# Performance work log

Hardware: AMD Instinct MI355X
Metric: run time of the kernel (lower is better)

The kernel has to match this reference:

```python
import jax, jax.numpy as jnp
import numpy as np
import math

B, SEQ, E, H, NB, NHYP = 4, 1024, 512, 8, 64, 6
V, HID, NC, ENC = 32000, 2048, 6, 6
DH = E // H


def _pos_encoding(n, e, dtype):
    pos = jnp.arange(n, dtype=dtype)[:, None]
    div = jnp.exp(-jnp.arange(0, e, 2, dtype=dtype) * (math.log(10000.0) / e))
    ang = pos * div  # [n, e/2]
    pe = jnp.zeros((n, e), dtype)
    pe = pe.at[:, 0::2].set(jnp.sin(ang))
    pe = pe.at[:, 1::2].set(jnp.cos(ang))
    return pe


def _layer_norm(x, g, b):
    m = x.mean(-1, keepdims=True)
    v = ((x - m) ** 2).mean(-1, keepdims=True)
    return (x - m) / jnp.sqrt(v + 1e-5) * g + b


def _lsh_attention(x, Wq, bq, Wv, bv, hyper):
    b, n, e = x.shape
    q = x @ Wq + bq
    v = x @ Wv + bv
    q4 = q.reshape(b, n, H, DH)  # [b,n,h,d]
    v4 = v.reshape(b, n, H, DH)
    # bucket hashing: append bias 1, project on hyperplanes, binarize, binary-encode
    aug = jnp.concatenate([q4, jnp.ones((b, n, H, 1), q.dtype)], axis=-1)
    proj = jnp.einsum('bnhe,ey->bnhy', aug, hyper)
    bits = (proj >= 0).astype(q.dtype)
    pows = (2 ** jnp.arange(NHYP)).astype(q.dtype)
    buckets = jnp.einsum('bnhy,y->bnh', bits, pows).astype(jnp.int32)
    bh = buckets.transpose(0, 2, 1)  # [b,h,n]
    qh = q4.transpose(0, 2, 1, 3)  # [b,h,n,d]
    vh = v4.transpose(0, 2, 1, 3)
    scores = jnp.einsum('bhnd,bhmd->bhnm', qh, qh) / math.sqrt(e)
    # torch code zeroes q rows at their OWN bucket and sums q_c @ q_c^T over all
    # NB buckets; that equals scores * (NB - 2 + [bucket_i == bucket_j]) exactly.
    same = bh[:, :, :, None] == bh[:, :, None, :]
    count = (NB - 2 + same.astype(jnp.int32)).astype(scores.dtype)
    attn = jax.nn.softmax(scores * count, axis=-1)
    out = jnp.einsum('bhnm,bhmd->bhnd', attn, vh)
    return out.transpose(0, 2, 1, 3).reshape(b, n, e)


def setup_inputs() -> dict:
    key = jax.random.key(0)
    ks = jax.random.split(key, 16)
    s = 0.02
    emb = jax.random.normal(ks[0], (V, E), jnp.float32) * s
    emb = emb.at[V - 1].set(0.0)  # padding_idx row
    return dict(
        inputs=jax.random.randint(ks[1], (B, SEQ), 0, V),
        emb=emb,
        gamma=jnp.ones((E,), jnp.float32),
        beta=jnp.zeros((E,), jnp.float32),
        Wq=jax.random.normal(ks[2], (E, E), jnp.float32) * s,
        bq=jnp.zeros((E,), jnp.float32),
        Wv=jax.random.normal(ks[3], (E, E), jnp.float32) * s,
        bv=jnp.zeros((E,), jnp.float32),
        hyper=jax.random.normal(ks[4], (DH + 1, NHYP), jnp.float32),
        W1=jax.random.normal(ks[5], (E, HID), jnp.float32) * s,
        b1=jnp.zeros((HID,), jnp.float32),
        W2=jax.random.normal(ks[6], (HID, E), jnp.float32) * s,
        b2=jnp.zeros((E,), jnp.float32),
        Wm=jax.random.normal(ks[7], (E * SEQ, NC), jnp.float32) * 0.002,
        bm=jnp.zeros((NC,), jnp.float32),
    )


def reference(inputs, emb, gamma, beta, Wq, bq, Wv, bv, hyper, W1, b1, W2, b2, Wm, bm):
    x = emb[inputs]  # [B, SEQ, E]
    x = x + _pos_encoding(x.shape[1], x.shape[2], x.dtype)
    for _ in range(ENC):  # shared weights across encoders
        a = _lsh_attention(x, Wq, bq, Wv, bv, hyper)
        x = _layer_norm(a, gamma, beta)
        x = jax.nn.relu(x @ W1 + b1) @ W2 + b2 + x
        x = _layer_norm(x, gamma, beta)
    x = x.reshape(x.shape[0], -1)
    return x @ Wm + bm  # [B, NC]
```

## Files before the change

kernel.cpp:

```cpp
#include <hip/hip_runtime.h>
#include <hip/hip_bf16.h>
#include <math.h>

#define B_    4
#define SEQ_  1024
#define E_    512
#define H_    8
#define DH_   64
#define NHYP_ 6
#define HID_  2048
#define NC_   6
#define ENC_  6
#define BH_   (B_*H_)
#define NTOK_ 4096
#define NCAT_ 1088

typedef __attribute__((ext_vector_type(8))) short short8;
typedef __attribute__((ext_vector_type(4))) float f32x4;

static __device__ __forceinline__ float wave_rsum(float v){
#pragma unroll
  for(int o=32;o;o>>=1) v += __shfl_down(v,o,64);
  return v;
}
static __device__ __forceinline__ ushort f2b(float v){
  __hip_bfloat16 h = __float2bfloat16(v);
  return *(ushort*)&h;
}
static __device__ __forceinline__ float b2f(ushort u){
  unsigned int x = ((unsigned int)u) << 16;
  return *(float*)&x;
}
static __device__ __forceinline__ void gload16(const void* g, void* l){
  __builtin_amdgcn_global_load_lds(
      (const __attribute__((address_space(1))) void*)g,
      (__attribute__((address_space(3))) void*)l,
      16, 0, 0);
}

__global__ void embed_pe_kernel(const int* __restrict__ inp, const float* __restrict__ emb,
                                float* __restrict__ x, ushort* __restrict__ xh,
                                unsigned int* __restrict__ MaxN){
  int row = blockIdx.x;
  if(blockIdx.x==0 && threadIdx.x<32) MaxN[threadIdx.x] = 0u;
  int s = row & (SEQ_-1);
  int idx = inp[row];
  const float* er = emb + (size_t)idx*E_;
  float* xr = x + (size_t)row*E_;
  ushort* hr = xh + (size_t)row*E_;
  for(int c=threadIdx.x;c<E_;c+=blockDim.x){
    int i = c>>1;
    float div = expf(-(float)i * 0.0359778920780319646f);
    float ang = (float)s * div;
    float pe = (c&1) ? cosf(ang) : sinf(ang);
    float v = er[c] + pe;
    xr[c] = v;
    hr[c] = f2b(v);
  }
}

__global__ __launch_bounds__(256) void prep_kernel(
    const float* __restrict__ Wq, const float* __restrict__ Wv,
    const float* __restrict__ W1, const float* __restrict__ W2,
    const float* __restrict__ bq, const float* __restrict__ bv,
    const float* __restrict__ hyper,
    ushort* __restrict__ WcatT, ushort* __restrict__ W1T,
    ushort* __restrict__ W2T, float* __restrict__ bcat)
{
  int bid = blockIdx.x;
  if(bid < 2560){
    const float* W; ushort* Wt; int K, N, tile;
    if(bid < 256){       W=Wq; Wt=WcatT;                    K=512;  N=512;  tile=bid; }
    else if(bid < 512){  W=Wv; Wt=WcatT+(size_t)512*512;    K=512;  N=512;  tile=bid-256; }
    else if(bid < 1536){ W=W1; Wt=W1T;                      K=512;  N=2048; tile=bid-512; }
    else {               W=W2; Wt=W2T;                      K=2048; N=512;  tile=bid-1536; }
    int tpr = N >> 5;
    int n0 = (tile % tpr)*32, k0 = (tile / tpr)*32;
    __shared__ float T[32][33];
    int tx = threadIdx.x & 31, ty = threadIdx.x >> 5;
#pragma unroll
    for(int i=0;i<32;i+=8) T[ty+i][tx] = W[(size_t)(k0+ty+i)*N + n0+tx];
    __syncthreads();
#pragma unroll
    for(int i=0;i<32;i+=8)
      Wt[(size_t)(n0+ty+i)*K + k0+tx] = f2b(T[tx][ty+i]);
  } else if(bid < 2688){
    int t = (bid-2560)*256 + threadIdx.x;
    int c = t >> 9, k = t & 511;
    float s = 0.f;
    if(c < 48){
      int h = c/6, y = c%6;
      const float* wr = Wq + (size_t)k*E_ + h*DH_;
      for(int d=0;d<DH_;++d) s += wr[d]*hyper[d*NHYP_+y];
    }
    WcatT[(size_t)(1024+c)*E_ + k] = f2b(s);
  } else {
    int t = (bid-2688)*256 + threadIdx.x;
    if(t >= NCAT_) return;
    float v;
    if(t < 512) v = bq[t];
    else if(t < 1024) v = bv[t-512];
    else if(t < 1072){
      int c = t - 1024, h = c/6, y = c%6;
      float s = hyper[DH_*NHYP_ + y];
      for(int d=0;d<DH_;++d) s += bq[h*DH_+d]*hyper[d*NHYP_+y];
      v = s;
    } else v = 0.f;
    bcat[t] = v;
  }
}

template<int BM, int BN, int EPI>
__global__ __launch_bounds__(256) void gemm_mfma(
    const ushort* __restrict__ A, const ushort* __restrict__ Bt,
    const float* __restrict__ bias, const float* __restrict__ res,
    void* __restrict__ C0, void* __restrict__ C1, void* __restrict__ C2,
    void* __restrict__ C3, int M, int N, int K)
{
  constexpr int MI = BM/32, NI = BN/32;
  constexpr int ACH = BM/32, BCH = BN/32;
  __shared__ ushort As[2][BM*64];
  __shared__ ushort Bs[2][BN*64];
  __shared__ float epi[64*49];
  int tid = threadIdx.x;
  int w = tid>>6, lane = tid&63, g = lane>>4, li = lane&15;
  int wr = w>>1, wc = w&1;
  int bm = blockIdx.y*BM, bn = blockIdx.x*BN;
  int kz = blockIdx.z;
  int kcnt = K / (int)gridDim.z;
  int kbase = kz * kcnt;
  int NK = kcnt >> 6;

  f32x4 acc[MI][NI] = {};

  auto issue = [&](int ks, int pb){
    int k0 = kbase + ks*64;
#pragma unroll
    for(int it=0; it<ACH; ++it){
      int c = it*256 + tid; int r = c>>3; int kq = ((c&7)^(r&7))*8;
      gload16(&A[(size_t)(bm+r)*K + k0 + kq], &As[pb][it*2048 + w*512]);
    }
#pragma unroll
    for(int it=0; it<BCH; ++it){
      int c = it*256 + tid; int r = c>>3; int kq = ((c&7)^(r&7))*8;
      gload16(&Bt[(size_t)(bn+r)*K + k0 + kq], &Bs[pb][it*2048 + w*512]);
    }
  };

  issue(0, 0);
  __syncthreads();
  for(int ks=0; ks<NK; ++ks){
    if(ks+1 < NK) issue(ks+1, (ks+1)&1);
    int pb = ks&1;
#pragma unroll
    for(int kc=0; kc<2; ++kc){
      short8 af[MI], bf[NI];
#pragma unroll
      for(int mi=0;mi<MI;++mi)
        af[mi] = *(const short8*)&As[pb][(wr*(BM/2)+mi*16+li)*64 + (((kc*4+g)^(li&7))*8)];
#pragma unroll
      for(int ni=0;ni<NI;++ni)
        bf[ni] = *(const short8*)&Bs[pb][(wc*(BN/2)+ni*16+li)*64 + (((kc*4+g)^(li&7))*8)];
#pragma unroll
      for(int mi=0;mi<MI;++mi)
#pragma unroll
        for(int ni=0;ni<NI;++ni)
          acc[mi][ni] = __builtin_amdgcn_mfma_f32_16x16x32_bf16(af[mi], bf[ni], acc[mi][ni], 0,0,0);
    }
    __syncthreads();
  }

  if(EPI==5){
    if(bn < 512){
      int h = bn >> 6;
#pragma unroll
      for(int mi=0;mi<MI;++mi){
        int rbase = bm + wr*(BM/2) + mi*16 + g*4;
        float q2s[4] = {0.f,0.f,0.f,0.f};
#pragma unroll
        for(int ni=0;ni<NI;++ni){
          int cc = bn + wc*(BN/2) + ni*16 + li;
          float bv = bias[cc];
          int d = cc & 63;
#pragma unroll
          for(int j=0;j<4;++j){
            float vvf = acc[mi][ni][j] + bv;
            ushort ub = f2b(vvf);
            int r = rbase + j; int b = r>>10, n = r&1023;
            ((ushort*)C1)[(((size_t)(b*8+h))*1024 + n)*64 + d] = ub;
            float f = b2f(ub);
            q2s[j] += f*f;
          }
        }
#pragma unroll
        for(int j=0;j<4;++j){
#pragma unroll
          for(int o=8;o;o>>=1) q2s[j] += __shfl_xor(q2s[j], o, 64);
        }
        if(li==0){
#pragma unroll
          for(int j=0;j<4;++j)
            epi[(wr*(BM/2)+mi*16+g*4+j)*2 + wc] = q2s[j];
        }
      }
      __syncthreads();
      if(tid < 64){
        int r = bm + tid; int b = r>>10, n = r&1023;
        float q2 = epi[tid*2] + epi[tid*2+1];
        ((float*)C3)[((size_t)(b*8+h))*1024 + n] = q2;
        float m = q2;
#pragma unroll
        for(int o=32;o;o>>=1) m = fmaxf(m, __shfl_xor(m, o, 64));
        if(tid==0){
          int bh = (bm>>10)*8 + h;
          atomicMax((unsigned int*)res + bh, __float_as_uint(m));
        }
      }
    } else if(bn < 1024){
#pragma unroll
      for(int mi=0;mi<MI;++mi){
        int rbase = bm + wr*(BM/2) + mi*16 + g*4;
        int b = rbase>>10, n = rbase&1023;
#pragma unroll
        for(int ni=0;ni<NI;++ni){
          int cc = bn + wc*(BN/2) + ni*16 + li;
          float bv = bias[cc];
          int cl = cc - 512; int h = cl>>6, d = cl&63;
          ushort4 pk;
          pk.x = f2b(acc[mi][ni][0]+bv); pk.y = f2b(acc[mi][ni][1]+bv);
          pk.z = f2b(acc[mi][ni][2]+bv); pk.w = f2b(acc[mi][ni][3]+bv);
          *(ushort4*)&((ushort*)C2)[(((size_t)(b*8+h))*64 + d)*1024 + n] = pk;
        }
      }
    } else {
#pragma unroll
      for(int mi=0;mi<MI;++mi){
        int rloc = wr*(BM/2) + mi*16 + g*4;
#pragma unroll
        for(int ni=0;ni<NI;++ni){
          int c = wc*(BN/2) + ni*16 + li;
          if(c < 48){
            float bv = bias[1024 + c];
#pragma unroll
            for(int j=0;j<4;++j)
              epi[(rloc+j)*49 + c] = acc[mi][ni][j] + bv;
          }
        }
      }
      __syncthreads();
      if(tid < 64){
        int r = bm + tid; int b = r>>10, n = r&1023;
#pragma unroll
        for(int h=0;h<8;++h){
          int bk = 0;
#pragma unroll
          for(int y=0;y<NHYP_;++y)
            bk |= (epi[tid*49 + h*NHYP_ + y] >= 0.0f) ? (1<<y) : 0;
          ((int*)C0)[((size_t)(b*8+h))*1024 + n] = bk;
        }
      }
    }
    return;
  }

#pragma unroll
  for(int mi=0;mi<MI;++mi){
    int rbase = bm + wr*(BM/2) + mi*16 + g*4;
#pragma unroll
    for(int ni=0;ni<NI;++ni){
      int cc = bn + wc*(BN/2) + ni*16 + li;
      float bv = (EPI==6) ? 0.0f : bias[cc];
      float vv[4];
#pragma unroll
      for(int j=0;j<4;++j) vv[j] = acc[mi][ni][j] + bv;
      if(EPI==1){
#pragma unroll
        for(int j=0;j<4;++j) ((ushort*)C0)[(size_t)(rbase+j)*N + cc] = f2b(fmaxf(vv[j],0.0f));
      } else if(EPI==6){
        float* dst = (float*)C0 + (size_t)kz*M*N;
#pragma unroll
        for(int j=0;j<4;++j) dst[(size_t)(rbase+j)*N + cc] = vv[j];
      } else if(EPI==2){
#pragma unroll
        for(int j=0;j<4;++j){
          size_t o = (size_t)(rbase+j)*N + cc;
          ((float*)C0)[o] = vv[j] + res[o];
        }
      } else {
#pragma unroll
        for(int j=0;j<4;++j) ((float*)C0)[(size_t)(rbase+j)*N + cc] = vv[j];
      }
    }
  }
}

__global__ __launch_bounds__(256) void attn_mfma_kernel(
    const ushort* __restrict__ Qh,
    const ushort* __restrict__ Vt,
    const int* __restrict__ buckets,
    const float* __restrict__ qn2,
    const unsigned int* __restrict__ MaxN,
    float* __restrict__ outp)
{
  int bid = blockIdx.x;
  int bh = bid & 31;
  int qt = bid >> 5;
  int b = bh >> 3, h = bh & 7;
  int tid = threadIdx.x;
  int w = tid >> 6, lane = tid & 63;
  int g = lane >> 4, li = lane & 15;

  __shared__ ushort Ks[2][64*64];
  __shared__ ushort Vs[2][64*64];
  __shared__ ushort Ps[64*68];
  __shared__ int bks[2][64];
  __shared__ int bqs[64];

  const ushort* Qbase = Qh + (size_t)bh*SEQ_*DH_;
  const ushort* Vbase = Vt + (size_t)bh*DH_*SEQ_;
  const int* Bb = buckets + bh*SEQ_;
  const float* qn = qn2 + bh*SEQ_;
  int q0 = qt*64;

  auto issue = [&](int kt, int pb){
    int j0 = kt*64;
#pragma unroll
    for(int it=0; it<2; ++it){
      int c = it*256 + tid; int r = c>>3; int ks = ((c&7)^(r&7))*8;
      gload16(&Qbase[(size_t)(j0+r)*DH_ + ks], &Ks[pb][it*2048 + w*512]);
      gload16(&Vbase[(size_t)r*SEQ_ + j0 + ks], &Vs[pb][it*2048 + w*512]);
    }
    if(tid < 16) gload16(&Bb[j0 + tid*4], &bks[pb][0]);
  };

  issue(0, 0);
  short8 qa[2];
  int qrow = q0 + w*16 + li;
#pragma unroll
  for(int kc=0; kc<2; ++kc)
    qa[kc] = *(const short8*)&Qbase[(size_t)qrow*DH_ + kc*32 + g*8];
  if(tid < 64) bqs[tid] = Bb[q0 + tid];

  float maxn = sqrtf(__uint_as_float(MaxN[bh]));

  const float invsq = 0.04419417382415922f;
  const float LOG2E = 1.4426950408889634f;
  const float c62l = invsq * 62.0f * LOG2E;
  const float c63l = invsq * 63.0f * LOG2E;
  float nM2[4];
#pragma unroll
  for(int i=0;i<4;++i){
    float Mrow = invsq*63.0f * sqrtf(qn[q0 + w*16 + g*4 + i]) * maxn + 1.0f;
    nM2[i] = -Mrow * LOG2E;
  }
  __syncthreads();

  f32x4 acc_o[4] = {};
  float psum[4] = {0.f,0.f,0.f,0.f};

  for(int kt=0; kt<16; ++kt){
    if(kt < 15) issue(kt+1, (kt+1)&1);
    int pb = kt&1;

    f32x4 accs[4];
    __builtin_amdgcn_s_setprio(1);
#pragma unroll
    for(int nt=0; nt<4; ++nt){
      f32x4 z = {};
#pragma unroll
      for(int kc=0; kc<2; ++kc){
        short8 kb = *(const short8*)&Ks[pb][(nt*16+li)*64 + (((kc*4+g)^(li&7))*8)];
        z = __builtin_amdgcn_mfma_f32_16x16x32_bf16(qa[kc], kb, z, 0,0,0);
      }
      accs[nt] = z;
    }
    __builtin_amdgcn_s_setprio(0);
    int bkc[4];
#pragma unroll
    for(int nt=0;nt<4;++nt) bkc[nt] = bks[pb][nt*16 + li];

#pragma unroll
    for(int i=0;i<4;++i){
      int rloc = w*16 + g*4 + i;
      int bq = bqs[rloc];
      float rs = 0.f;
#pragma unroll
      for(int nt=0;nt<4;++nt){
        float cl = (bkc[nt] == bq) ? c63l : c62l;
        float e = exp2f(fmaf(accs[nt][i], cl, nM2[i]));
        rs += e;
        Ps[rloc*68 + nt*16 + li] = f2b(e);
      }
      psum[i] += rs;
    }
    __builtin_amdgcn_s_setprio(1);
#pragma unroll
    for(int dt=0; dt<4; ++dt){
      f32x4 z = acc_o[dt];
#pragma unroll
      for(int kc=0; kc<2; ++kc){
        short8 pa = *(const short8*)&Ps[(w*16+li)*68 + kc*32 + g*8];
        short8 vb = *(const short8*)&Vs[pb][(dt*16+li)*64 + (((kc*4+g)^(li&7))*8)];
        z = __builtin_amdgcn_mfma_f32_16x16x32_bf16(pa, vb, z, 0,0,0);
      }
      acc_o[dt] = z;
    }
    __builtin_amdgcn_s_setprio(0);
    __syncthreads();
  }
#pragma unroll
  for(int i=0;i<4;++i){
#pragma unroll
    for(int o=8;o;o>>=1) psum[i] += __shfl_xor(psum[i], o, 64);
  }
  float* obase = outp + ((size_t)(b*SEQ_ + q0 + w*16 + g*4))*E_ + h*DH_;
#pragma unroll
  for(int i=0;i<4;++i){
    float inv = 1.0f / fmaxf(psum[i], 1e-35f);
#pragma unroll
    for(int dt=0;dt<4;++dt)
      obase[(size_t)i*E_ + dt*16 + li] = acc_o[dt][i] * inv;
  }
}

__global__ __launch_bounds__(256) void ln_kernel(
    const float* __restrict__ in, const float* __restrict__ g,
    const float* __restrict__ bb, float* __restrict__ outp,
    ushort* __restrict__ oh, unsigned int* __restrict__ MaxN){
  if(blockIdx.x==0 && threadIdx.x<32) MaxN[threadIdx.x] = 0u;
  int row = blockIdx.x*4 + (threadIdx.x>>6);
  int lane = threadIdx.x & 63;
  const float4* xr = (const float4*)(in + (size_t)row*E_);
  float4 v0 = xr[lane*2], v1 = xr[lane*2+1];
  float s  = v0.x+v0.y+v0.z+v0.w + v1.x+v1.y+v1.z+v1.w;
  float s2 = v0.x*v0.x+v0.y*v0.y+v0.z*v0.z+v0.w*v0.w
           + v1.x*v1.x+v1.y*v1.y+v1.z*v1.z+v1.w*v1.w;
#pragma unroll
  for(int o=32;o;o>>=1){ s += __shfl_xor(s,o,64); s2 += __shfl_xor(s2,o,64); }
  float mean = s*(1.0f/E_);
  float var  = s2*(1.0f/E_) - mean*mean;
  float inv = rsqrtf(var + 1e-5f);
  const float4* g4 = (const float4*)(g) + lane*2;
  const float4* b4 = (const float4*)(bb) + lane*2;
  float4 g0 = g4[0], g1 = g4[1], b0 = b4[0], b1 = b4[1];
  float4 y0, y1;
  y0.x=(v0.x-mean)*inv*g0.x+b0.x; y0.y=(v0.y-mean)*inv*g0.y+b0.y;
  y0.z=(v0.z-mean)*inv*g0.z+b0.z; y0.w=(v0.w-mean)*inv*g0.w+b0.w;
  y1.x=(v1.x-mean)*inv*g1.x+b1.x; y1.y=(v1.y-mean)*inv*g1.y+b1.y;
  y1.z=(v1.z-mean)*inv*g1.z+b1.z; y1.w=(v1.w-mean)*inv*g1.w+b1.w;
  float4* orow = (float4*)(outp + (size_t)row*E_) + lane*2;
  orow[0] = y0; orow[1] = y1;
  ushort hs[8];
  hs[0]=f2b(y0.x); hs[1]=f2b(y0.y); hs[2]=f2b(y0.z); hs[3]=f2b(y0.w);
  hs[4]=f2b(y1.x); hs[5]=f2b(y1.y); hs[6]=f2b(y1.z); hs[7]=f2b(y1.w);
  *(uint4*)&oh[(size_t)row*E_ + lane*8] = *(uint4*)hs;
}

__global__ __launch_bounds__(256) void ln2_kernel(
    const float* __restrict__ P, const float* __restrict__ b2,
    const float* __restrict__ Xres, const float* __restrict__ g,
    const float* __restrict__ bb, float* __restrict__ outp,
    ushort* __restrict__ oh){
  int row = blockIdx.x*4 + (threadIdx.x>>6);
  int lane = threadIdx.x & 63;
  const float4* p0 = (const float4*)(P + (size_t)row*E_) + lane*2;
  const float4* p1 = (const float4*)(P + (size_t)NTOK_*E_ + (size_t)row*E_) + lane*2;
  const float4* xr = (const float4*)(Xres + (size_t)row*E_) + lane*2;
  const float4* c4 = (const float4*)(b2) + lane*2;
  float4 v0 = p0[0], v1 = p0[1], u0 = p1[0], u1 = p1[1];
  float4 x0 = xr[0], x1 = xr[1], cb0 = c4[0], cb1 = c4[1];
  v0.x += u0.x + cb0.x + x0.x; v0.y += u0.y + cb0.y + x0.y;
  v0.z += u0.z + cb0.z + x0.z; v0.w += u0.w + cb0.w + x0.w;
  v1.x += u1.x + cb1.x + x1.x; v1.y += u1.y + cb1.y + x1.y;
  v1.z += u1.z + cb1.z + x1.z; v1.w += u1.w + cb1.w + x1.w;
  float s  = v0.x+v0.y+v0.z+v0.w + v1.x+v1.y+v1.z+v1.w;
  float s2 = v0.x*v0.x+v0.y*v0.y+v0.z*v0.z+v0.w*v0.w
           + v1.x*v1.x+v1.y*v1.y+v1.z*v1.z+v1.w*v1.w;
#pragma unroll
  for(int o=32;o;o>>=1){ s += __shfl_xor(s,o,64); s2 += __shfl_xor(s2,o,64); }
  float mean = s*(1.0f/E_);
  float var  = s2*(1.0f/E_) - mean*mean;
  float inv = rsqrtf(var + 1e-5f);
  const float4* g4 = (const float4*)(g) + lane*2;
  const float4* b4 = (const float4*)(bb) + lane*2;
  float4 g0 = g4[0], g1 = g4[1], b0 = b4[0], b1 = b4[1];
  float4 y0, y1;
  y0.x=(v0.x-mean)*inv*g0.x+b0.x; y0.y=(v0.y-mean)*inv*g0.y+b0.y;
  y0.z=(v0.z-mean)*inv*g0.z+b0.z; y0.w=(v0.w-mean)*inv*g0.w+b0.w;
  y1.x=(v1.x-mean)*inv*g1.x+b1.x; y1.y=(v1.y-mean)*inv*g1.y+b1.y;
  y1.z=(v1.z-mean)*inv*g1.z+b1.z; y1.w=(v1.w-mean)*inv*g1.w+b1.w;
  float4* orow = (float4*)(outp + (size_t)row*E_) + lane*2;
  orow[0] = y0; orow[1] = y1;
  ushort hs[8];
  hs[0]=f2b(y0.x); hs[1]=f2b(y0.y); hs[2]=f2b(y0.z); hs[3]=f2b(y0.w);
  hs[4]=f2b(y1.x); hs[5]=f2b(y1.y); hs[6]=f2b(y1.z); hs[7]=f2b(y1.w);
  *(uint4*)&oh[(size_t)row*E_ + lane*8] = *(uint4*)hs;
}

__global__ void final_partial(const float* __restrict__ x, const float* __restrict__ Wm,
                              float* __restrict__ part){
  int b  = blockIdx.x >> 7;
  int ch = blockIdx.x & 127;
  const float* xb = x + (size_t)b*SEQ_*E_;
  int k0 = ch*4096;
  float acc[NC_] = {};
  for(int k=k0+threadIdx.x; k<k0+4096; k+=256){
    float xv = xb[k];
    const float* wrow = Wm + (size_t)k*NC_;
#pragma unroll
    for(int c=0;c<NC_;++c) acc[c] += xv*wrow[c];
  }
#pragma unroll
  for(int c=0;c<NC_;++c) acc[c] = wave_rsum(acc[c]);
  __shared__ float r[4][NC_];
  int w = threadIdx.x>>6, lane = threadIdx.x&63;
  if(lane==0){
#pragma unroll
    for(int c=0;c<NC_;++c) r[w][c] = acc[c];
  }
  __syncthreads();
  if(threadIdx.x==0){
#pragma unroll
    for(int c=0;c<NC_;++c)
      part[(size_t)blockIdx.x*NC_ + c] = r[0][c]+r[1][c]+r[2][c]+r[3][c];
  }
}

__global__ void final_reduce(const float* __restrict__ part, const float* __restrict__ bm,
                             float* __restrict__ out){
  int t = threadIdx.x;
  if(t >= B_*NC_) return;
  int b = t / NC_, c = t % NC_;
  float s = bm[c];
  for(int i=0;i<128;++i) s += part[(size_t)(b*128+i)*NC_ + c];
  out[t] = s;
}

extern "C" void kernel_launch(void* const* d_in, const int* in_sizes, int n_in,
                              void* d_out, int out_size, void* d_ws, size_t ws_size,
                              hipStream_t stream){
  const int*   inp   = (const int*)d_in[0];
  const float* emb   = (const float*)d_in[1];
  const float* gamma = (const float*)d_in[2];
  const float* beta  = (const float*)d_in[3];
  const float* Wq    = (const float*)d_in[4];
  const float* bq    = (const float*)d_in[5];
  const float* Wv    = (const float*)d_in[6];
  const float* bv    = (const float*)d_in[7];
  const float* hyper = (const float*)d_in[8];
  const float* W1    = (const float*)d_in[9];
  const float* b1    = (const float*)d_in[10];
  const float* W2    = (const float*)d_in[11];
  const float* b2    = (const float*)d_in[12];
  const float* Wm    = (const float*)d_in[13];
  const float* bm    = (const float*)d_in[14];
  float* out = (float*)d_out;

  char* ws = (char*)d_ws;
  size_t off = 0;
  auto alloc = [&](size_t bytes)->void*{
    void* p = ws + off; off += (bytes + 255) & ~(size_t)255; return p;
  };
  const size_t NTOK = (size_t)B_*SEQ_;
  float*  X    = (float*)alloc(NTOK*E_*sizeof(float));
  float*  A    = (float*)alloc(NTOK*E_*sizeof(float));
  float*  Op   = (float*)alloc((size_t)2*NTOK*E_*sizeof(float));
  ushort* Xh   = (ushort*)alloc(NTOK*E_*sizeof(ushort));
  ushort* Hh   = (ushort*)alloc(NTOK*HID_*sizeof(ushort));
  int*    Bk   = (int*)  alloc((size_t)BH_*SEQ_*sizeof(int));
  float*  Qn2  = (float*)alloc((size_t)BH_*SEQ_*sizeof(float));
  unsigned int* MaxN = (unsigned int*)alloc(32*sizeof(unsigned int));
  float*  Pp   = (float*)alloc((size_t)B_*128*NC_*sizeof(float));
  ushort* Qh   = (ushort*)alloc((size_t)BH_*SEQ_*DH_*sizeof(ushort));
  ushort* Vt   = (ushort*)alloc((size_t)BH_*DH_*SEQ_*sizeof(ushort));
  ushort* WcatT= (ushort*)alloc((size_t)NCAT_*E_*sizeof(ushort));
  ushort* W1T  = (ushort*)alloc((size_t)HID_*E_*sizeof(ushort));
  ushort* W2T  = (ushort*)alloc((size_t)E_*HID_*sizeof(ushort));
  float*  bcat = (float*)alloc(NCAT_*sizeof(float));
  (void)ws_size; (void)in_sizes; (void)n_in; (void)out_size;

  prep_kernel<<<2693, 256, 0, stream>>>(Wq, Wv, W1, W2, bq, bv, hyper,
                                        WcatT, W1T, W2T, bcat);
  embed_pe_kernel<<<B_*SEQ_, 256, 0, stream>>>(inp, emb, X, Xh, MaxN);

  dim3 gQV(NCAT_/64, (B_*SEQ_)/64);
  dim3 gF1(HID_/128, (B_*SEQ_)/128);
  dim3 gF2(E_/64,    (B_*SEQ_)/64, 2);
  for(int l=0;l<ENC_;++l){
    gemm_mfma<64,64,5><<<gQV, 256, 0, stream>>>(Xh, WcatT, bcat, (const float*)MaxN,
                                                Bk, Qh, Vt, Qn2, B_*SEQ_, NCAT_, E_);
    attn_mfma_kernel<<<BH_*16, 256, 0, stream>>>(Qh, Vt, Bk, Qn2, MaxN, A);
    ln_kernel<<<B_*SEQ_/4, 256, 0, stream>>>(A, gamma, beta, X, Xh, MaxN);
    gemm_mfma<128,128,1><<<gF1, 256, 0, stream>>>(Xh, W1T, b1, nullptr, Hh, nullptr, nullptr, nullptr, B_*SEQ_, HID_, E_);
    gemm_mfma<64,64,6><<<gF2, 256, 0, stream>>>(Hh, W2T, b2, nullptr, Op, nullptr, nullptr, nullptr, B_*SEQ_, E_, HID_);
    ln2_kernel<<<B_*SEQ_/4, 256, 0, stream>>>(Op, b2, X, gamma, beta, X, Xh);
  }
  final_partial<<<B_*128, 256, 0, stream>>>(X, Wm, Pp);
  final_reduce<<<1, 32, 0, stream>>>(Pp, bm, out);
}
```

Measured before the change: 596.5 us.

## Fuse both layer norms into producer kernels via last-block atomic counters

Removes the two standalone layer-norm kernels per encoder layer. The attention kernel and the split-K FFN2 GEMM now count finished blocks per row tile with atomic counters, and the last block to finish runs the residual add and layer norm for those 64 rows. The counters are reset inside the QKV GEMM epilogue, and the MaxN reset moves into the fused FFN2 path. This saves two launches and some memory round trips per layer. In exchange it adds threadfences and atomics, and the layer-norm work is serialized onto a few late blocks.

```diff
diff --git a/kernel.cpp b/kernel.cpp
--- a/kernel.cpp
+++ b/kernel.cpp
@@ -36,6 +36,34 @@
       (const __attribute__((address_space(1))) void*)g,
       (__attribute__((address_space(3))) void*)l,
       16, 0, 0);
+}
+
+static __device__ __forceinline__ void ln_row_store(
+    float4 v0, float4 v1, const float* g, const float* bb,
+    float* outp, ushort* oh, size_t row, int lane)
+{
+  float s  = v0.x+v0.y+v0.z+v0.w + v1.x+v1.y+v1.z+v1.w;
+  float s2 = v0.x*v0.x+v0.y*v0.y+v0.z*v0.z+v0.w*v0.w
+           + v1.x*v1.x+v1.y*v1.y+v1.z*v1.z+v1.w*v1.w;
+#pragma unroll
+  for(int o=32;o;o>>=1){ s += __shfl_xor(s,o,64); s2 += __shfl_xor(s2,o,64); }
+  float mean = s*(1.0f/E_);
+  float var  = s2*(1.0f/E_) - mean*mean;
+  float inv = rsqrtf(var + 1e-5f);
+  const float4* g4 = (const float4*)(g) + lane*2;
+  const float4* b4 = (const float4*)(bb) + lane*2;
+  float4 g0 = g4[0], g1 = g4[1], b0 = b4[0], b1 = b4[1];
+  float4 y0, y1;
+  y0.x=(v0.x-mean)*inv*g0.x+b0.x; y0.y=(v0.y-mean)*inv*g0.y+b0.y;
+  y0.z=(v0.z-mean)*inv*g0.z+b0.z; y0.w=(v0.w-mean)*inv*g0.w+b0.w;
+  y1.x=(v1.x-mean)*inv*g1.x+b1.x; y1.y=(v1.y-mean)*inv*g1.y+b1.y;
+  y1.z=(v1.z-mean)*inv*g1.z+b1.z; y1.w=(v1.w-mean)*inv*g1.w+b1.w;
+  float4* orow = (float4*)(outp + row*E_) + lane*2;
+  orow[0] = y0; orow[1] = y1;
+  ushort hs[8];
+  hs[0]=f2b(y0.x); hs[1]=f2b(y0.y); hs[2]=f2b(y0.z); hs[3]=f2b(y0.w);
+  hs[4]=f2b(y1.x); hs[5]=f2b(y1.y); hs[6]=f2b(y1.z); hs[7]=f2b(y1.w);
+  *(uint4*)&oh[row*E_ + lane*8] = *(uint4*)hs;
 }
 
 __global__ void embed_pe_kernel(const int* __restrict__ inp, const float* __restrict__ emb,
@@ -115,13 +143,16 @@
     const ushort* __restrict__ A, const ushort* __restrict__ Bt,
     const float* __restrict__ bias, const float* __restrict__ res,
     void* __restrict__ C0, void* __restrict__ C1, void* __restrict__ C2,
-    void* __restrict__ C3, int M, int N, int K)
+    void* __restrict__ C3, const float* __restrict__ lng,
+    const float* __restrict__ lnb, int* __restrict__ Ctr,
+    int M, int N, int K)
 {
   constexpr int MI = BM/32, NI = BN/32;
   constexpr int ACH = BM/32, BCH = BN/32;
   __shared__ ushort As[2][BM*64];
   __shared__ ushort Bs[2][BN*64];
   __shared__ float epi[64*49];
+  __shared__ int lastf;
   int tid = threadIdx.x;
   int w = tid>>6, lane = tid&63, g = lane>>4, li = lane&15;
   int wr = w>>1, wc = w&1;
@@ -233,6 +264,7 @@
         }
       }
     } else {
+      if(tid < 2) Ctr[(bm>>6) + tid*64] = 0;
 #pragma unroll
       for(int mi=0;mi<MI;++mi){
         int rloc = wr*(BM/2) + mi*16 + g*4;
@@ -280,15 +312,31 @@
         float* dst = (float*)C0 + (size_t)kz*M*N;
 #pragma unroll
         for(int j=0;j<4;++j) dst[(size_t)(rbase+j)*N + cc] = vv[j];
-      } else if(EPI==2){
-#pragma unroll
-        for(int j=0;j<4;++j){
-          size_t o = (size_t)(rbase+j)*N + cc;
-          ((float*)C0)[o] = vv[j] + res[o];
-        }
-      } else {
-#pragma unroll
-        for(int j=0;j<4;++j) ((float*)C0)[(size_t)(rbase+j)*N + cc] = vv[j];
+      }
+    }
+  }
+
+  if(EPI==6){
+    __threadfence();
+    __syncthreads();
+    if(tid==0) lastf = (atomicAdd(&Ctr[64 + (bm>>6)], 1) == 15);
+    __syncthreads();
+    if(lastf){
+      __threadfence();
+      if((bm>>6)==0 && tid<32) ((unsigned int*)C2)[tid] = 0u;
+      for(int rr=w; rr<64; rr+=4){
+        size_t row = (size_t)bm + rr;
+        const float4* p0 = (const float4*)((const float*)C0 + row*N) + lane*2;
+        const float4* p1 = (const float4*)((const float*)C0 + (size_t)M*N + row*N) + lane*2;
+        const float4* xr = (const float4*)(res + row*N) + lane*2;
+        const float4* c4 = (const float4*)bias + lane*2;
+        float4 v0=p0[0], v1=p0[1], u0=p1[0], u1=p1[1];
+        float4 x0=xr[0], x1=xr[1], cb0=c4[0], cb1=c4[1];
+        v0.x += u0.x + cb0.x + x0.x; v0.y += u0.y + cb0.y + x0.y;
+        v0.z += u0.z + cb0.z + x0.z; v0.w += u0.w + cb0.w + x0.w;
+        v1.x += u1.x + cb1.x + x1.x; v1.y += u1.y + cb1.y + x1.y;
+        v1.z += u1.z + cb1.z + x1.z; v1.w += u1.w + cb1.w + x1.w;
+        ln_row_store(v0, v1, lng, lnb, (float*)C3, (ushort*)C1, row, lane);
       }
     }
   }
@@ -300,7 +348,10 @@
     const int* __restrict__ buckets,
     const float* __restrict__ qn2,
     const unsigned int* __restrict__ MaxN,
-    float* __restrict__ outp)
+    float* __restrict__ outp,
+    float* __restrict__ X, ushort* __restrict__ Xh,
+    const float* __restrict__ lng, const float* __restrict__ lnb,
+    int* __restrict__ Ctr)
 {
   int bid = blockIdx.x;
   int bh = bid & 31;
@@ -315,6 +366,7 @@
   __shared__ ushort Ps[64*68];
   __shared__ int bks[2][64];
   __shared__ int bqs[64];
+  __shared__ int lastf;
 
   const ushort* Qbase = Qh + (size_t)bh*SEQ_*DH_;
   const ushort* Vbase = Vt + (size_t)bh*DH_*SEQ_;
@@ -421,80 +473,21 @@
     for(int dt=0;dt<4;++dt)
       obase[(size_t)i*E_ + dt*16 + li] = acc_o[dt][i] * inv;
   }
-}
-
-__global__ __launch_bounds__(256) void ln_kernel(
-    const float* __restrict__ in, const float* __restrict__ g,
-    const float* __restrict__ bb, float* __restrict__ outp,
-    ushort* __restrict__ oh, unsigned int* __restrict__ MaxN){
-  if(blockIdx.x==0 && threadIdx.x<32) MaxN[threadIdx.x] = 0u;
-  int row = blockIdx.x*4 + (threadIdx.x>>6);
-  int lane = threadIdx.x & 63;
-  const float4* xr = (const float4*)(in + (size_t)row*E_);
-  float4 v0 = xr[lane*2], v1 = xr[lane*2+1];
-  float s  = v0.x+v0.y+v0.z+v0.w + v1.x+v1.y+v1.z+v1.w;
-  float s2 = v0.x*v0.x+v0.y*v0.y+v0.z*v0.z+v0.w*v0.w
-           + v1.x*v1.x+v1.y*v1.y+v1.z*v1.z+v1.w*v1.w;
-#pragma unroll
-  for(int o=32;o;o>>=1){ s += __shfl_xor(s,o,64); s2 += __shfl_xor(s2,o,64); }
-  float mean = s*(1.0f/E_);
-  float var  = s2*(1.0f/E_) - mean*mean;
-  float inv = rsqrtf(var + 1e-5f);
-  const float4* g4 = (const float4*)(g) + lane*2;
-  const float4* b4 = (const float4*)(bb) + lane*2;
-  float4 g0 = g4[0], g1 = g4[1], b0 = b4[0], b1 = b4[1];
-  float4 y0, y1;
-  y0.x=(v0.x-mean)*inv*g0.x+b0.x; y0.y=(v0.y-mean)*inv*g0.y+b0.y;
-  y0.z=(v0.z-mean)*inv*g0.z+b0.z; y0.w=(v0.w-mean)*inv*g0.w+b0.w;
-  y1.x=(v1.x-mean)*inv*g1.x+b1.x; y1.y=(v1.y-mean)*inv*g1.y+b1.y;
-  y1.z=(v1.z-mean)*inv*g1.z+b1.z; y1.w=(v1.w-mean)*inv*g1.w+b1.w;
-  float4* orow = (float4*)(outp + (size_t)row*E_) + lane*2;
-  orow[0] = y0; orow[1] = y1;
-  ushort hs[8];
-  hs[0]=f2b(y0.x); hs[1]=f2b(y0.y); hs[2]=f2b(y0.z); hs[3]=f2b(y0.w);
-  hs[4]=f2b(y1.x); hs[5]=f2b(y1.y); hs[6]=f2b(y1.z); hs[7]=f2b(y1.w);
-  *(uint4*)&oh[(size_t)row*E_ + lane*8] = *(uint4*)hs;
-}
-
-__global__ __launch_bounds__(256) void ln2_kernel(
-    const float* __restrict__ P, const float* __restrict__ b2,
-    const float* __restrict__ Xres, const float* __restrict__ g,
-    const float* __restrict__ bb, float* __restrict__ outp,
-    ushort* __restrict__ oh){
-  int row = blockIdx.x*4 + (threadIdx.x>>6);
-  int lane = threadIdx.x & 63;
-  const float4* p0 = (const float4*)(P + (size_t)row*E_) + lane*2;
-  const float4* p1 = (const float4*)(P + (size_t)NTOK_*E_ + (size_t)row*E_) + lane*2;
-  const float4* xr = (const float4*)(Xres + (size_t)row*E_) + lane*2;
-  const float4* c4 = (const float4*)(b2) + lane*2;
-  float4 v0 = p0[0], v1 = p0[1], u0 = p1[0], u1 = p1[1];
-  float4 x0 = xr[0], x1 = xr[1], cb0 = c4[0], cb1 = c4[1];
-  v0.x += u0.x + cb0.x + x0.x; v0.y += u0.y + cb0.y + x0.y;
-  v0.z += u0.z + cb0.z + x0.z; v0.w += u0.w + cb0.w + x0.w;
-  v1.x += u1.x + cb1.x + x1.x; v1.y += u1.y + cb1.y + x1.y;
-  v1.z += u1.z + cb1.z + x1.z; v1.w += u1.w + cb1.w + x1.w;
-  float s  = v0.x+v0.y+v0.z+v0.w + v1.x+v1.y+v1.z+v1.w;
-  float s2 = v0.x*v0.x+v0.y*v0.y+v0.z*v0.z+v0.w*v0.w
-           + v1.x*v1.x+v1.y*v1.y+v1.z*v1.z+v1.w*v1.w;
-#pragma unroll
-  for(int o=32;o;o>>=1){ s += __shfl_xor(s,o,64); s2 += __shfl_xor(s2,o,64); }
-  float mean = s*(1.0f/E_);
-  float var  = s2*(1.0f/E_) - mean*mean;
-  float inv = rsqrtf(var + 1e-5f);
-  const float4* g4 = (const float4*)(g) + lane*2;
-  const float4* b4 = (const float4*)(bb) + lane*2;
-  float4 g0 = g4[0], g1 = g4[1], b0 = b4[0], b1 = b4[1];
-  float4 y0, y1;
-  y0.x=(v0.x-mean)*inv*g0.x+b0.x; y0.y=(v0.y-mean)*inv*g0.y+b0.y;
-  y0.z=(v0.z-mean)*inv*g0.z+b0.z; y0.w=(v0.w-mean)*inv*g0.w+b0.w;
-  y1.x=(v1.x-mean)*inv*g1.x+b1.x; y1.y=(v1.y-mean)*inv*g1.y+b1.y;
-  y1.z=(v1.z-mean)*inv*g1.z+b1.z; y1.w=(v1.w-mean)*inv*g1.w+b1.w;
-  float4* orow = (float4*)(outp + (size_t)row*E_) + lane*2;
-  orow[0] = y0; orow[1] = y1;
-  ushort hs[8];
-  hs[0]=f2b(y0.x); hs[1]=f2b(y0.y); hs[2]=f2b(y0.z); hs[3]=f2b(y0.w);
-  hs[4]=f2b(y1.x); hs[5]=f2b(y1.y); hs[6]=f2b(y1.z); hs[7]=f2b(y1.w);
-  *(uint4*)&oh[(size_t)row*E_ + lane*8] = *(uint4*)hs;
+
+  __threadfence();
+  __syncthreads();
+  if(tid==0) lastf = (atomicAdd(&Ctr[b*16 + qt], 1) == 7);
+  __syncthreads();
+  if(lastf){
+    __threadfence();
+    size_t rowbase = (size_t)b*SEQ_ + q0;
+    for(int rr=w; rr<64; rr+=4){
+      size_t row = rowbase + rr;
+      const float4* xr = (const float4*)(outp + row*E_) + lane*2;
+      float4 v0 = xr[0], v1 = xr[1];
+      ln_row_store(v0, v1, lng, lnb, X, Xh, row, lane);
+    }
+  }
 }
 
 __global__ void final_partial(const float* __restrict__ x, const float* __restrict__ Wm,
@@ -570,6 +563,7 @@
   int*    Bk   = (int*)  alloc((size_t)BH_*SEQ_*sizeof(int));
   float*  Qn2  = (float*)alloc((size_t)BH_*SEQ_*sizeof(float));
   unsigned int* MaxN = (unsigned int*)alloc(32*sizeof(unsigned int));
+  int*    Ctr  = (int*)alloc(128*sizeof(int));
   float*  Pp   = (float*)alloc((size_t)B_*128*NC_*sizeof(float));
   ushort* Qh   = (ushort*)alloc((size_t)BH_*SEQ_*DH_*sizeof(ushort));
   ushort* Vt   = (ushort*)alloc((size_t)BH_*DH_*SEQ_*sizeof(ushort));
@@ -587,13 +581,17 @@
   dim3 gF1(HID_/128, (B_*SEQ_)/128);
   dim3 gF2(E_/64,    (B_*SEQ_)/64, 2);
   for(int l=0;l<ENC_;++l){
-    gemm_mfma<64,64,5><<<gQV, 256, 0, stream>>>(Xh, WcatT, bcat, (const float*)MaxN,
-                                                Bk, Qh, Vt, Qn2, B_*SEQ_, NCAT_, E_);
-    attn_mfma_kernel<<<BH_*16, 256, 0, stream>>>(Qh, Vt, Bk, Qn2, MaxN, A);
-    ln_kernel<<<B_*SEQ_/4, 256, 0, stream>>>(A, gamma, beta, X, Xh, MaxN);
-    gemm_mfma<128,128,1><<<gF1, 256, 0, stream>>>(Xh, W1T, b1, nullptr, Hh, nullptr, nullptr, nullptr, B_*SEQ_, HID_, E_);
-    gemm_mfma<64,64,6><<<gF2, 256, 0, stream>>>(Hh, W2T, b2, nullptr, Op, nullptr, nullptr, nullptr, B_*SEQ_, E_, HID_);
-    ln2_kernel<<<B_*SEQ_/4, 256, 0, stream>>>(Op, b2, X, gamma, beta, X, Xh);
+    gemm_mfma<64,64,5><<<gQV, 256, 0, stream>>>(
+        Xh, WcatT, bcat, (const float*)MaxN,
+        Bk, Qh, Vt, Qn2, nullptr, nullptr, Ctr, B_*SEQ_, NCAT_, E_);
+    attn_mfma_kernel<<<BH_*16, 256, 0, stream>>>(
+        Qh, Vt, Bk, Qn2, MaxN, A, X, Xh, gamma, beta, Ctr);
+    gemm_mfma<128,128,1><<<gF1, 256, 0, stream>>>(
+        Xh, W1T, b1, nullptr, Hh, nullptr, nullptr, nullptr,
+        nullptr, nullptr, nullptr, B_*SEQ_, HID_, E_);
+    gemm_mfma<64,64,6><<<gF2, 256, 0, stream>>>(
+        Hh, W2T, b2, X, Op, Xh, (void*)MaxN, X,
+        gamma, beta, Ctr, B_*SEQ_, E_, HID_);
   }
   final_partial<<<B_*128, 256, 0, stream>>>(X, Wm, Pp);
   final_reduce<<<1, 32, 0, stream>>>(Pp, bm, out);
```

New measurement: 2.037 ms. +241.5%, slower.

## Fold first LayerNorm into FFN1 GEMM via gamma-scaled weights and row statistics

Applied to the files above, without the earlier changes.

Removes the standalone LayerNorm kernel after attention. Attention now writes bf16 output, and FFN1 runs directly on the raw attention output using W1 pre-scaled by gamma. Per-row mean and inverse std are computed in the GEMM prologue and applied in the epilogue as inv*acc - mean*inv*gw1 + cw1. The second LN kernel recomputes the first LN's output from the bf16 attention output to form the residual. This saves one kernel launch plus fp32 read/write traffic per layer, at the cost of some precision (bf16 activations, single-pass variance) and redundant statistics work in every column tile.

```diff
diff --git a/kernel.cpp b/kernel.cpp
--- a/kernel.cpp
+++ b/kernel.cpp
@@ -63,16 +63,18 @@
     const float* __restrict__ Wq, const float* __restrict__ Wv,
     const float* __restrict__ W1, const float* __restrict__ W2,
     const float* __restrict__ bq, const float* __restrict__ bv,
-    const float* __restrict__ hyper,
-    ushort* __restrict__ WcatT, ushort* __restrict__ W1T,
-    ushort* __restrict__ W2T, float* __restrict__ bcat)
+    const float* __restrict__ b1, const float* __restrict__ hyper,
+    const float* __restrict__ gamma, const float* __restrict__ beta,
+    ushort* __restrict__ WcatT, ushort* __restrict__ W1gT,
+    ushort* __restrict__ W2T, float* __restrict__ bcat,
+    float* __restrict__ gw1, float* __restrict__ cw1)
 {
   int bid = blockIdx.x;
   if(bid < 2560){
-    const float* W; ushort* Wt; int K, N, tile;
+    const float* W; ushort* Wt; int K, N, tile; bool scale = false;
     if(bid < 256){       W=Wq; Wt=WcatT;                    K=512;  N=512;  tile=bid; }
     else if(bid < 512){  W=Wv; Wt=WcatT+(size_t)512*512;    K=512;  N=512;  tile=bid-256; }
-    else if(bid < 1536){ W=W1; Wt=W1T;                      K=512;  N=2048; tile=bid-512; }
+    else if(bid < 1536){ W=W1; Wt=W1gT;                     K=512;  N=2048; tile=bid-512; scale=true; }
     else {               W=W2; Wt=W2T;                      K=2048; N=512;  tile=bid-1536; }
     int tpr = N >> 5;
     int n0 = (tile % tpr)*32, k0 = (tile / tpr)*32;
@@ -81,9 +83,10 @@
 #pragma unroll
     for(int i=0;i<32;i+=8) T[ty+i][tx] = W[(size_t)(k0+ty+i)*N + n0+tx];
     __syncthreads();
+    float gs = scale ? gamma[k0+tx] : 1.0f;
 #pragma unroll
     for(int i=0;i<32;i+=8)
-      Wt[(size_t)(n0+ty+i)*K + k0+tx] = f2b(T[tx][ty+i]);
+      Wt[(size_t)(n0+ty+i)*K + k0+tx] = f2b(gs * T[tx][ty+i]);
   } else if(bid < 2688){
     int t = (bid-2560)*256 + threadIdx.x;
     int c = t >> 9, k = t & 511;
@@ -94,7 +97,7 @@
       for(int d=0;d<DH_;++d) s += wr[d]*hyper[d*NHYP_+y];
     }
     WcatT[(size_t)(1024+c)*E_ + k] = f2b(s);
-  } else {
+  } else if(bid < 2693){
     int t = (bid-2688)*256 + threadIdx.x;
     if(t >= NCAT_) return;
     float v;
@@ -107,6 +110,16 @@
       v = s;
     } else v = 0.f;
     bcat[t] = v;
+  } else {
+    int n = (bid-2693)*256 + threadIdx.x;
+    float s1 = 0.f, s2 = 0.f;
+    for(int k=0;k<E_;++k){
+      float w = W1[(size_t)k*HID_ + n];
+      s1 += gamma[k]*w;
+      s2 += beta[k]*w;
+    }
+    gw1[n] = s1;
+    cw1[n] = s2 + b1[n];
   }
 }
 
@@ -148,6 +161,29 @@
   };
 
   issue(0, 0);
+
+  if(EPI==7){
+    for(int i=0;i<BM/4;++i){
+      int rr = w*(BM/4) + i;
+      short8 v = *(const short8*)&A[(size_t)(bm+rr)*K + lane*8];
+      float s = 0.f, s2 = 0.f;
+#pragma unroll
+      for(int j=0;j<8;++j){
+        float f = b2f((ushort)v[j]);
+        s += f; s2 += f*f;
+      }
+#pragma unroll
+      for(int o=32;o;o>>=1){ s += __shfl_xor(s,o,64); s2 += __shfl_xor(s2,o,64); }
+      if(lane==0){
+        float mean = s*(1.0f/E_);
+        float var  = s2*(1.0f/E_) - mean*mean;
+        float inv = rsqrtf(var + 1e-5f);
+        epi[rr] = mean*inv;
+        epi[BM+rr] = inv;
+      }
+    }
+  }
+
   __syncthreads();
   for(int ks=0; ks<NK; ++ks){
     if(ks+1 < NK) issue(ks+1, (ks+1)&1);
@@ -269,26 +305,19 @@
 #pragma unroll
     for(int ni=0;ni<NI;++ni){
       int cc = bn + wc*(BN/2) + ni*16 + li;
-      float bv = (EPI==6) ? 0.0f : bias[cc];
-      float vv[4];
-#pragma unroll
-      for(int j=0;j<4;++j) vv[j] = acc[mi][ni][j] + bv;
-      if(EPI==1){
-#pragma unroll
-        for(int j=0;j<4;++j) ((ushort*)C0)[(size_t)(rbase+j)*N + cc] = f2b(fmaxf(vv[j],0.0f));
-      } else if(EPI==6){
+      if(EPI==7){
+        float gwv = res[cc];
+        float cwv = bias[cc];
+#pragma unroll
+        for(int j=0;j<4;++j){
+          int rloc = wr*(BM/2) + mi*16 + g*4 + j;
+          float vvf = epi[BM+rloc]*acc[mi][ni][j] - epi[rloc]*gwv + cwv;
+          ((ushort*)C0)[(size_t)(rbase+j)*N + cc] = f2b(fmaxf(vvf, 0.0f));
+        }
+      } else {
         float* dst = (float*)C0 + (size_t)kz*M*N;
 #pragma unroll
-        for(int j=0;j<4;++j) dst[(size_t)(rbase+j)*N + cc] = vv[j];
-      } else if(EPI==2){
-#pragma unroll
-        for(int j=0;j<4;++j){
-          size_t o = (size_t)(rbase+j)*N + cc;
-          ((float*)C0)[o] = vv[j] + res[o];
-        }
-      } else {
-#pragma unroll
-        for(int j=0;j<4;++j) ((float*)C0)[(size_t)(rbase+j)*N + cc] = vv[j];
+        for(int j=0;j<4;++j) dst[(size_t)(rbase+j)*N + cc] = acc[mi][ni][j];
       }
     }
   }
@@ -300,7 +329,7 @@
     const int* __restrict__ buckets,
     const float* __restrict__ qn2,
     const unsigned int* __restrict__ MaxN,
-    float* __restrict__ outp)
+    ushort* __restrict__ Ah)
 {
   int bid = blockIdx.x;
   int bh = bid & 31;
@@ -413,25 +442,55 @@
 #pragma unroll
     for(int o=8;o;o>>=1) psum[i] += __shfl_xor(psum[i], o, 64);
   }
-  float* obase = outp + ((size_t)(b*SEQ_ + q0 + w*16 + g*4))*E_ + h*DH_;
+  ushort* obase = Ah + ((size_t)(b*SEQ_ + q0 + w*16 + g*4))*E_ + h*DH_;
 #pragma unroll
   for(int i=0;i<4;++i){
     float inv = 1.0f / fmaxf(psum[i], 1e-35f);
 #pragma unroll
     for(int dt=0;dt<4;++dt)
-      obase[(size_t)i*E_ + dt*16 + li] = acc_o[dt][i] * inv;
-  }
-}
-
-__global__ __launch_bounds__(256) void ln_kernel(
-    const float* __restrict__ in, const float* __restrict__ g,
+      obase[(size_t)i*E_ + dt*16 + li] = f2b(acc_o[dt][i] * inv);
+  }
+}
+
+__global__ __launch_bounds__(256) void ln2_kernel(
+    const float* __restrict__ P, const float* __restrict__ b2,
+    const ushort* __restrict__ Ah, const float* __restrict__ g,
     const float* __restrict__ bb, float* __restrict__ outp,
     ushort* __restrict__ oh, unsigned int* __restrict__ MaxN){
   if(blockIdx.x==0 && threadIdx.x<32) MaxN[threadIdx.x] = 0u;
   int row = blockIdx.x*4 + (threadIdx.x>>6);
   int lane = threadIdx.x & 63;
-  const float4* xr = (const float4*)(in + (size_t)row*E_);
-  float4 v0 = xr[lane*2], v1 = xr[lane*2+1];
+  const float4* g4 = (const float4*)(g) + lane*2;
+  const float4* b4 = (const float4*)(bb) + lane*2;
+  float4 g0 = g4[0], g1 = g4[1], b0 = b4[0], b1v = b4[1];
+
+  short8 av = *(const short8*)&Ah[(size_t)row*E_ + lane*8];
+  float a[8];
+  float as = 0.f, as2 = 0.f;
+#pragma unroll
+  for(int j=0;j<8;++j){
+    a[j] = b2f((ushort)av[j]);
+    as += a[j]; as2 += a[j]*a[j];
+  }
+#pragma unroll
+  for(int o=32;o;o>>=1){ as += __shfl_xor(as,o,64); as2 += __shfl_xor(as2,o,64); }
+  float am = as*(1.0f/E_);
+  float ainv = rsqrtf(as2*(1.0f/E_) - am*am + 1e-5f);
+  float rg[8];
+  rg[0]=(a[0]-am)*ainv*g0.x+b0.x; rg[1]=(a[1]-am)*ainv*g0.y+b0.y;
+  rg[2]=(a[2]-am)*ainv*g0.z+b0.z; rg[3]=(a[3]-am)*ainv*g0.w+b0.w;
+  rg[4]=(a[4]-am)*ainv*g1.x+b1v.x; rg[5]=(a[5]-am)*ainv*g1.y+b1v.y;
+  rg[6]=(a[6]-am)*ainv*g1.z+b1v.z; rg[7]=(a[7]-am)*ainv*g1.w+b1v.w;
+
+  const float4* p0 = (const float4*)(P + (size_t)row*E_) + lane*2;
+  const float4* p1 = (const float4*)(P + (size_t)NTOK_*E_ + (size_t)row*E_) + lane*2;
+  const float4* c4 = (const float4*)(b2) + lane*2;
+  float4 v0 = p0[0], v1 = p0[1], u0 = p1[0], u1 = p1[1];
+  float4 cb0 = c4[0], cb1 = c4[1];
+  v0.x += u0.x + cb0.x + rg[0]; v0.y += u0.y + cb0.y + rg[1];
+  v0.z += u0.z + cb0.z + rg[2]; v0.w += u0.w + cb0.w + rg[3];
+  v1.x += u1.x + cb1.x + rg[4]; v1.y += u1.y + cb1.y + rg[5];
+  v1.z += u1.z + cb1.z + rg[6]; v1.w += u1.w + cb1.w + rg[7];
   float s  = v0.x+v0.y+v0.z+v0.w + v1.x+v1.y+v1.z+v1.w;
   float s2 = v0.x*v0.x+v0.y*v0.y+v0.z*v0.z+v0.w*v0.w
            + v1.x*v1.x+v1.y*v1.y+v1.z*v1.z+v1.w*v1.w;
@@ -440,55 +499,11 @@
   float mean = s*(1.0f/E_);
   float var  = s2*(1.0f/E_) - mean*mean;
   float inv = rsqrtf(var + 1e-5f);
-  const float4* g4 = (const float4*)(g) + lane*2;
-  const float4* b4 = (const float4*)(bb) + lane*2;
-  float4 g0 = g4[0], g1 = g4[1], b0 = b4[0], b1 = b4[1];
   float4 y0, y1;
   y0.x=(v0.x-mean)*inv*g0.x+b0.x; y0.y=(v0.y-mean)*inv*g0.y+b0.y;
   y0.z=(v0.z-mean)*inv*g0.z+b0.z; y0.w=(v0.w-mean)*inv*g0.w+b0.w;
-  y1.x=(v1.x-mean)*inv*g1.x+b1.x; y1.y=(v1.y-mean)*inv*g1.y+b1.y;
-  y1.z=(v1.z-mean)*inv*g1.z+b1.z; y1.w=(v1.w-mean)*inv*g1.w+b1.w;
-  float4* orow = (float4*)(outp + (size_t)row*E_) + lane*2;
-  orow[0] = y0; orow[1] = y1;
-  ushort hs[8];
-  hs[0]=f2b(y0.x); hs[1]=f2b(y0.y); hs[2]=f2b(y0.z); hs[3]=f2b(y0.w);
-  hs[4]=f2b(y1.x); hs[5]=f2b(y1.y); hs[6]=f2b(y1.z); hs[7]=f2b(y1.w);
-  *(uint4*)&oh[(size_t)row*E_ + lane*8] = *(uint4*)hs;
-}
-
-__global__ __launch_bounds__(256) void ln2_kernel(
-    const float* __restrict__ P, const float* __restrict__ b2,
-    const float* __restrict__ Xres, const float* __restrict__ g,
-    const float* __restrict__ bb, float* __restrict__ outp,
-    ushort* __restrict__ oh){
-  int row = blockIdx.x*4 + (threadIdx.x>>6);
-  int lane = threadIdx.x & 63;
-  const float4* p0 = (const float4*)(P + (size_t)row*E_) + lane*2;
-  const float4* p1 = (const float4*)(P + (size_t)NTOK_*E_ + (size_t)row*E_) + lane*2;
-  const float4* xr = (const float4*)(Xres + (size_t)row*E_) + lane*2;
-  const float4* c4 = (const float4*)(b2) + lane*2;
-  float4 v0 = p0[0], v1 = p0[1], u0 = p1[0], u1 = p1[1];
-  float4 x0 = xr[0], x1 = xr[1], cb0 = c4[0], cb1 = c4[1];
-  v0.x += u0.x + cb0.x + x0.x; v0.y += u0.y + cb0.y + x0.y;
-  v0.z += u0.z + cb0.z + x0.z; v0.w += u0.w + cb0.w + x0.w;
-  v1.x += u1.x + cb1.x + x1.x; v1.y += u1.y + cb1.y + x1.y;
-  v1.z += u1.z + cb1.z + x1.z; v1.w += u1.w + cb1.w + x1.w;
-  float s  = v0.x+v0.y+v0.z+v0.w + v1.x+v1.y+v1.z+v1.w;
-  float s2 = v0.x*v0.x+v0.y*v0.y+v0.z*v0.z+v0.w*v0.w
-           + v1.x*v1.x+v1.y*v1.y+v1.z*v1.z+v1.w*v1.w;
-#pragma unroll
-  for(int o=32;o;o>>=1){ s += __shfl_xor(s,o,64); s2 += __shfl_xor(s2,o,64); }
-  float mean = s*(1.0f/E_);
-  float var  = s2*(1.0f/E_) - mean*mean;
-  float inv = rsqrtf(var + 1e-5f);
-  const float4* g4 = (const float4*)(g) + lane*2;
-  const float4* b4 = (const float4*)(bb) + lane*2;
-  float4 g0 = g4[0], g1 = g4[1], b0 = b4[0], b1 = b4[1];
-  float4 y0, y1;
-  y0.x=(v0.x-mean)*inv*g0.x+b0.x; y0.y=(v0.y-mean)*inv*g0.y+b0.y;
-  y0.z=(v0.z-mean)*inv*g0.z+b0.z; y0.w=(v0.w-mean)*inv*g0.w+b0.w;
-  y1.x=(v1.x-mean)*inv*g1.x+b1.x; y1.y=(v1.y-mean)*inv*g1.y+b1.y;
-  y1.z=(v1.z-mean)*inv*g1.z+b1.z; y1.w=(v1.w-mean)*inv*g1.w+b1.w;
+  y1.x=(v1.x-mean)*inv*g1.x+b1v.x; y1.y=(v1.y-mean)*inv*g1.y+b1v.y;
+  y1.z=(v1.z-mean)*inv*g1.z+b1v.z; y1.w=(v1.w-mean)*inv*g1.w+b1v.w;
   float4* orow = (float4*)(outp + (size_t)row*E_) + lane*2;
   orow[0] = y0; orow[1] = y1;
   ushort hs[8];
@@ -563,7 +578,7 @@
   };
   const size_t NTOK = (size_t)B_*SEQ_;
   float*  X    = (float*)alloc(NTOK*E_*sizeof(float));
-  float*  A    = (float*)alloc(NTOK*E_*sizeof(float));
+  ushort* Ah   = (ushort*)alloc(NTOK*E_*sizeof(ushort));
   float*  Op   = (float*)alloc((size_t)2*NTOK*E_*sizeof(float));
   ushort* Xh   = (ushort*)alloc(NTOK*E_*sizeof(ushort));
   ushort* Hh   = (ushort*)alloc(NTOK*HID_*sizeof(ushort));
@@ -574,13 +589,16 @@
   ushort* Qh   = (ushort*)alloc((size_t)BH_*SEQ_*DH_*sizeof(ushort));
   ushort* Vt   = (ushort*)alloc((size_t)BH_*DH_*SEQ_*sizeof(ushort));
   ushort* WcatT= (ushort*)alloc((size_t)NCAT_*E_*sizeof(ushort));
-  ushort* W1T  = (ushort*)alloc((size_t)HID_*E_*sizeof(ushort));
+  ushort* W1gT = (ushort*)alloc((size_t)HID_*E_*sizeof(ushort));
   ushort* W2T  = (ushort*)alloc((size_t)E_*HID_*sizeof(ushort));
   float*  bcat = (float*)alloc(NCAT_*sizeof(float));
+  float*  gw1  = (float*)alloc(HID_*sizeof(float));
+  float*  cw1  = (float*)alloc(HID_*sizeof(float));
   (void)ws_size; (void)in_sizes; (void)n_in; (void)out_size;
 
-  prep_kernel<<<2693, 256, 0, stream>>>(Wq, Wv, W1, W2, bq, bv, hyper,
-                                        WcatT, W1T, W2T, bcat);
+  prep_kernel<<<2701, 256, 0, stream>>>(Wq, Wv, W1, W2, bq, bv, b1, hyper,
+                                        gamma, beta, WcatT, W1gT, W2T, bcat,
+                                        gw1, cw1);
   embed_pe_kernel<<<B_*SEQ_, 256, 0, stream>>>(inp, emb, X, Xh, MaxN);
 
   dim3 gQV(NCAT_/64, (B_*SEQ_)/64);
@@ -589,11 +607,14 @@
   for(int l=0;l<ENC_;++l){
     gemm_mfma<64,64,5><<<gQV, 256, 0, stream>>>(Xh, WcatT, bcat, (const float*)MaxN,
                                                 Bk, Qh, Vt, Qn2, B_*SEQ_, NCAT_, E_);
-    attn_mfma_kernel<<<BH_*16, 256, 0, stream>>>(Qh, Vt, Bk, Qn2, MaxN, A);
-    ln_kernel<<<B_*SEQ_/4, 256, 0, stream>>>(A, gamma, beta, X, Xh, MaxN);
-    gemm_mfma<128,128,1><<<gF1, 256, 0, stream>>>(Xh, W1T, b1, nullptr, Hh, nullptr, nullptr, nullptr, B_*SEQ_, HID_, E_);
-    gemm_mfma<64,64,6><<<gF2, 256, 0, stream>>>(Hh, W2T, b2, nullptr, Op, nullptr, nullptr, nullptr, B_*SEQ_, E_, HID_);
-    ln2_kernel<<<B_*SEQ_/4, 256, 0, stream>>>(Op, b2, X, gamma, beta, X, Xh);
+    attn_mfma_kernel<<<BH_*16, 256, 0, stream>>>(Qh, Vt, Bk, Qn2, MaxN, Ah);
+    gemm_mfma<128,128,7><<<gF1, 256, 0, stream>>>(Ah, W1gT, cw1, gw1,
+                                                  Hh, nullptr, nullptr, nullptr,
+                                                  B_*SEQ_, HID_, E_);
+    gemm_mfma<64,64,6><<<gF2, 256, 0, stream>>>(Hh, W2T, b2, nullptr,
+                                                Op, nullptr, nullptr, nullptr,
+                                                B_*SEQ_, E_, HID_);
+    ln2_kernel<<<B_*SEQ_/4, 256, 0, stream>>>(Op, b2, Ah, gamma, beta, X, Xh, MaxN);
   }
   final_partial<<<B_*128, 256, 0, stream>>>(X, Wm, Pp);
   final_reduce<<<1, 32, 0, stream>>>(Pp, bm, out);
```

Measured after the change: 695.7 us. +16.6%, slower.
